# Optimization experiments

Measured on AMD Instinct MI355X. Metric: run time of the kernel, lower is better.

The kernel has to match this reference:

```python
import jax, jax.numpy as jnp
import numpy as np

GRID = (32, 32)       # SOM grid shape
INPUT_DIM = 512
BATCH = 16384
TAU = 0.5             # softmax temperature
EPS = 1e-8


def setup_inputs() -> dict:
    key = jax.random.key(0)
    k1, k2 = jax.random.split(key)
    x = jax.random.normal(k1, (BATCH, INPUT_DIM), dtype=jnp.float32)
    # glorot_uniform for shape (*GRID, INPUT_DIM): fan_in = 32*32, fan_out = 512
    fan_in, fan_out = GRID[0] * GRID[1], INPUT_DIM
    limit = float(np.sqrt(6.0 / (fan_in + fan_out)))
    weights_map = jax.random.uniform(
        k2, (*GRID, INPUT_DIM), dtype=jnp.float32, minval=-limit, maxval=limit
    )
    return {"x": x, "weights_map": weights_map}


def reference(x, weights_map):
    """SoftSOM forward: squared distances -> per-dimension softmax -> soft reconstruction."""
    B, D = x.shape
    gh, gw = GRID
    w_flat = weights_map.reshape(gh * gw, D)  # [N, D]
    d2 = (
        jnp.sum(x * x, axis=-1, keepdims=True)           # [B,1]
        + jnp.sum(w_flat * w_flat, axis=-1)[None, :]     # [1,N]
        - 2.0 * (x @ w_flat.T)                           # [B,N]
    )
    logits = (-d2 / TAU).reshape(B, gh, gw)
    # per-dimension softmax: softmax along each grid axis, combined multiplicatively
    s_rows = jax.nn.softmax(logits, axis=1)   # softmax over grid dim 0
    s_cols = jax.nn.softmax(logits, axis=2)   # softmax over grid dim 1
    a = s_rows * s_cols
    a = a / (jnp.sum(a, axis=(1, 2), keepdims=True) + EPS)  # renormalize over grid
    # soft reconstruction: weighted sum of prototypes
    y = jnp.einsum("bij,ijd->bd", a, weights_map)  # [B, D]
    return y
```

## Files before the change

### kernel.cpp

```cpp
#include <hip/hip_runtime.h>
#include <hip/hip_bf16.h>
#include <stdint.h>

#define B_SZ 16384
#define D_SZ 512
#define N_SZ 1024

using f16x8 = __attribute__((ext_vector_type(8))) _Float16;
using f32x4 = __attribute__((ext_vector_type(4))) float;

__device__ __forceinline__ unsigned short f16bits(_Float16 h) {
    return __builtin_bit_cast(unsigned short, h);
}

__global__ __launch_bounds__(256) void prep(
    const float* __restrict__ W, const float* __restrict__ X,
    _Float16* __restrict__ wh, _Float16* __restrict__ wt,
    float* __restrict__ ww, _Float16* __restrict__ xh) {
    const int bid = blockIdx.x;
    const int t = threadIdx.x;
    if (bid < 32) {
        __shared__ unsigned int cells[512 * 17];
        const int n0 = bid * 32;
        const int np = t >> 4;
        const int dc = t & 15;
        const int na = n0 + 2 * np, nb = na + 1;
        const int d0 = dc * 32;
        float va[32], vb[32];
#pragma unroll
        for (int i = 0; i < 8; ++i) {
            *reinterpret_cast<float4*>(&va[i * 4]) =
                *reinterpret_cast<const float4*>(&W[(size_t)na * D_SZ + d0 + i * 4]);
            *reinterpret_cast<float4*>(&vb[i * 4]) =
                *reinterpret_cast<const float4*>(&W[(size_t)nb * D_SZ + d0 + i * 4]);
        }
        float sa = 0.f, sb = 0.f;
#pragma unroll
        for (int i = 0; i < 32; ++i) { sa += va[i] * va[i]; sb += vb[i] * vb[i]; }
        sa += __shfl_xor(sa, 1); sa += __shfl_xor(sa, 2);
        sa += __shfl_xor(sa, 4); sa += __shfl_xor(sa, 8);
        sb += __shfl_xor(sb, 1); sb += __shfl_xor(sb, 2);
        sb += __shfl_xor(sb, 4); sb += __shfl_xor(sb, 8);
        if (dc == 0) { ww[na] = sa; ww[nb] = sb; }
        _Float16 ha[32], hb[32];
#pragma unroll
        for (int i = 0; i < 32; ++i) { ha[i] = (_Float16)va[i]; hb[i] = (_Float16)vb[i]; }
        unsigned int pa[16], pb[16];
#pragma unroll
        for (int j = 0; j < 16; ++j) {
            pa[j] = (unsigned)f16bits(ha[2 * j]) | ((unsigned)f16bits(ha[2 * j + 1]) << 16);
            pb[j] = (unsigned)f16bits(hb[2 * j]) | ((unsigned)f16bits(hb[2 * j + 1]) << 16);
        }
        unsigned int* whU = reinterpret_cast<unsigned int*>(wh);
#pragma unroll
        for (int j = 0; j < 4; ++j) {
            *reinterpret_cast<uint4*>(&whU[((size_t)na * D_SZ + d0) / 2 + j * 4]) =
                make_uint4(pa[j * 4], pa[j * 4 + 1], pa[j * 4 + 2], pa[j * 4 + 3]);
            *reinterpret_cast<uint4*>(&whU[((size_t)nb * D_SZ + d0) / 2 + j * 4]) =
                make_uint4(pb[j * 4], pb[j * 4 + 1], pb[j * 4 + 2], pb[j * 4 + 3]);
        }
#pragma unroll
        for (int k = 0; k < 32; ++k) {
            const int d = d0 + k;
            const unsigned u = (unsigned)f16bits(ha[k]) | ((unsigned)f16bits(hb[k]) << 16);
            cells[d * 17 + (np ^ ((d >> 5) & 15))] = u;
        }
        __syncthreads();
        for (int rr = 0; rr < 2; ++rr) {
            const int d = 2 * t + rr;
            const int px = (d >> 5) & 15;
            unsigned int buf[16];
#pragma unroll
            for (int j = 0; j < 16; ++j) buf[j] = cells[d * 17 + (j ^ px)];
            unsigned int* wtU = reinterpret_cast<unsigned int*>(wt);
#pragma unroll
            for (int j = 0; j < 4; ++j)
                *reinterpret_cast<uint4*>(&wtU[((size_t)d * N_SZ + n0) / 2 + j * 4]) =
                    make_uint4(buf[j * 4], buf[j * 4 + 1], buf[j * 4 + 2], buf[j * 4 + 3]);
        }
    } else {
        const int b2 = bid - 32;
        const int chunk = (b2 & 7) * 512 + (b2 >> 3);
        const size_t idx = ((size_t)chunk * 256 + t) * 8;
        const float4 a = *reinterpret_cast<const float4*>(&X[idx]);
        const float4 b = *reinterpret_cast<const float4*>(&X[idx + 4]);
        f16x8 h = {(_Float16)a.x, (_Float16)a.y, (_Float16)a.z, (_Float16)a.w,
                   (_Float16)b.x, (_Float16)b.y, (_Float16)b.z, (_Float16)b.w};
        *reinterpret_cast<f16x8*>(&xh[idx]) = h;
    }
}

__global__ __launch_bounds__(512, 2) void fused(
    const _Float16* __restrict__ xh, const _Float16* __restrict__ wh,
    const _Float16* __restrict__ wt, const float* __restrict__ ww,
    float* __restrict__ Y) {
    __shared__ __align__(16) char lds[152064];
    float* csw = (float*)lds;
    float* rs  = (float*)(lds + 131072);
    float* Mx  = (float*)(lds + 139264);
    float* Tw  = (float*)(lds + 141312);
    float* Mv  = (float*)(lds + 143360);
    float* Tv  = (float*)(lds + 143616);
    float* csf = (float*)(lds + 143872);

    const int tid = threadIdx.x;
    const int w = tid >> 6, l = tid & 63;
    const int l4 = l >> 4, lm = l & 15;
    const int raw = blockIdx.x;
    const int bm0 = ((raw & 7) * 32 + (raw >> 3)) * 64;

    f32x4 acc[4][8];
#pragma unroll
    for (int mi = 0; mi < 4; ++mi)
#pragma unroll
        for (int ni = 0; ni < 8; ++ni) acc[mi][ni] = (f32x4){0.f, 0.f, 0.f, 0.f};

    for (int kt = 0; kt < 16; ++kt) {
        const int gk = kt * 32;
        f16x8 af[4], bf[8];
#pragma unroll
        for (int mi = 0; mi < 4; ++mi)
            af[mi] = *reinterpret_cast<const f16x8*>(
                &xh[(size_t)(bm0 + mi * 16 + lm) * D_SZ + gk + l4 * 8]);
#pragma unroll
        for (int ni = 0; ni < 8; ++ni)
            bf[ni] = *reinterpret_cast<const f16x8*>(
                &wh[(size_t)(w * 128 + ni * 16 + lm) * D_SZ + gk + l4 * 8]);
#pragma unroll
        for (int mi = 0; mi < 4; ++mi)
#pragma unroll
            for (int ni = 0; ni < 8; ++ni)
                acc[mi][ni] = __builtin_amdgcn_mfma_f32_16x16x32_f16(af[mi], bf[ni], acc[mi][ni], 0, 0, 0);
    }
    float wwv[8];
#pragma unroll
    for (int ni = 0; ni < 8; ++ni) wwv[ni] = ww[w * 128 + ni * 16 + lm];
#pragma unroll
    for (int mi = 0; mi < 4; ++mi)
#pragma unroll
        for (int ni = 0; ni < 8; ++ni)
#pragma unroll
            for (int r = 0; r < 4; ++r)
                acc[mi][ni][r] = 4.f * acc[mi][ni][r] - 2.f * wwv[ni];

#pragma unroll
    for (int mi = 0; mi < 4; ++mi)
#pragma unroll
        for (int r = 0; r < 4; ++r) {
            float m = acc[mi][0][r];
#pragma unroll
            for (int ni = 1; ni < 8; ++ni) m = fmaxf(m, acc[mi][ni][r]);
            m = fmaxf(m, __shfl_xor(m, 1));
            m = fmaxf(m, __shfl_xor(m, 2));
            m = fmaxf(m, __shfl_xor(m, 4));
            m = fmaxf(m, __shfl_xor(m, 8));
            if (lm == 0) Mx[(mi * 16 + l4 * 4 + r) * 8 + w] = m;
        }
    __syncthreads();
    if (tid < 64) {
        float m = Mx[tid * 8];
#pragma unroll
        for (int k = 1; k < 8; ++k) m = fmaxf(m, Mx[tid * 8 + k]);
        Mv[tid] = m;
    }
    __syncthreads();
#pragma unroll
    for (int mi = 0; mi < 4; ++mi)
#pragma unroll
        for (int r = 0; r < 4; ++r) {
            const int b = mi * 16 + l4 * 4 + r;
            const float Mb = Mv[b];
            float u[8];
#pragma unroll
            for (int ni = 0; ni < 8; ++ni) {
                u[ni] = __expf(acc[mi][ni][r] - Mb);
                acc[mi][ni][r] = u[ni];
            }
#pragma unroll
            for (int ip = 0; ip < 4; ++ip) {
                float s = u[2 * ip] + u[2 * ip + 1];
                s += __shfl_xor(s, 1); s += __shfl_xor(s, 2);
                s += __shfl_xor(s, 4); s += __shfl_xor(s, 8);
                if (lm == 0) rs[b * 32 + 4 * w + ip] = s;
            }
#pragma unroll
            for (int jp = 0; jp < 2; ++jp) {
                const float c = (u[jp] + u[2 + jp]) + (u[4 + jp] + u[6 + jp]);
                csw[(w * 64 + b) * 32 + jp * 16 + lm] = c;
            }
        }
    __syncthreads();
    for (int c = tid; c < 2048; c += 512) {
        float s = csw[c];
#pragma unroll
        for (int k = 1; k < 8; ++k) s += csw[k * 2048 + c];
        csf[c] = s;
    }
    __syncthreads();
#pragma unroll
    for (int mi = 0; mi < 4; ++mi)
#pragma unroll
        for (int r = 0; r < 4; ++r) {
            const int b = mi * 16 + l4 * 4 + r;
            float rsv[4], csv[2];
#pragma unroll
            for (int ip = 0; ip < 4; ++ip) rsv[ip] = __builtin_amdgcn_rcpf(rs[b * 32 + 4 * w + ip]);
#pragma unroll
            for (int jp = 0; jp < 2; ++jp) csv[jp] = __builtin_amdgcn_rcpf(csf[b * 32 + jp * 16 + lm]);
            float tsum = 0.f;
#pragma unroll
            for (int ni = 0; ni < 8; ++ni) {
                const float uu = acc[mi][ni][r];
                const float t = uu * uu * rsv[ni >> 1] * csv[ni & 1];
                acc[mi][ni][r] = t;
                tsum += t;
            }
            tsum += __shfl_xor(tsum, 1); tsum += __shfl_xor(tsum, 2);
            tsum += __shfl_xor(tsum, 4); tsum += __shfl_xor(tsum, 8);
            if (lm == 0) Tw[b * 8 + w] = tsum;
        }
    __syncthreads();
    if (tid < 64) {
        float s = Tw[tid * 8];
#pragma unroll
        for (int k = 1; k < 8; ++k) s += Tw[tid * 8 + k];
        Tv[tid] = __builtin_amdgcn_rcpf(s + 1e-8f);
    }
    __syncthreads();
#pragma unroll
    for (int mi = 0; mi < 4; ++mi)
#pragma unroll
        for (int r = 0; r < 4; ++r) {
            const int b = mi * 16 + l4 * 4 + r;
            const float Tb = Tv[b];
#pragma unroll
            for (int ni = 0; ni < 8; ++ni) {
                const int n = w * 128 + ni * 16 + lm;
                const int off = b * 2048 + ((n * 2) ^ ((b & 7) << 4));
                *reinterpret_cast<_Float16*>(lds + off) = (_Float16)(acc[mi][ni][r] * Tb);
            }
        }
    __syncthreads();

    f32x4 acc2[4][4];
#pragma unroll
    for (int mi = 0; mi < 4; ++mi)
#pragma unroll
        for (int di = 0; di < 4; ++di) acc2[mi][di] = (f32x4){0.f, 0.f, 0.f, 0.f};

    for (int kt = 0; kt < 32; ++kt) {
        f16x8 a4[4], b4[4];
#pragma unroll
        for (int mi = 0; mi < 4; ++mi) {
            const int b = mi * 16 + lm;
            const int off = b * 2048 + ((kt * 64 + l4 * 16) ^ ((b & 7) << 4));
            a4[mi] = *reinterpret_cast<const f16x8*>(lds + off);
        }
#pragma unroll
        for (int di = 0; di < 4; ++di) {
            const int d = w * 64 + di * 16 + lm;
            b4[di] = *reinterpret_cast<const f16x8*>(
                &wt[(size_t)d * N_SZ + kt * 32 + l4 * 8]);
        }
#pragma unroll
        for (int mi = 0; mi < 4; ++mi)
#pragma unroll
            for (int di = 0; di < 4; ++di)
                acc2[mi][di] = __builtin_amdgcn_mfma_f32_16x16x32_f16(a4[mi], b4[di], acc2[mi][di], 0, 0, 0);
    }
#pragma unroll
    for (int mi = 0; mi < 4; ++mi)
#pragma unroll
        for (int di = 0; di < 4; ++di) {
            const int dd = w * 64 + di * 16 + lm;
            const int bb = bm0 + mi * 16 + l4 * 4;
#pragma unroll
            for (int r = 0; r < 4; ++r)
                Y[(size_t)(bb + r) * D_SZ + dd] = acc2[mi][di][r];
        }
}

extern "C" void kernel_launch(void* const* d_in, const int* in_sizes, int n_in,
                              void* d_out, int out_size, void* d_ws, size_t ws_size,
                              hipStream_t stream) {
    (void)in_sizes; (void)n_in; (void)out_size; (void)ws_size;
    const float* X = (const float*)d_in[0];
    const float* W = (const float*)d_in[1];
    float* Y = (float*)d_out;
    char* ws = (char*)d_ws;

    _Float16* wh = (_Float16*)ws;
    _Float16* wt = (_Float16*)(ws + (size_t)1 * 1024 * 1024);
    float*    ww = (float*)   (ws + (size_t)2 * 1024 * 1024);
    _Float16* xh = (_Float16*)(ws + (size_t)2 * 1024 * 1024 + 4096);

    prep<<<32 + 4096, 256, 0, stream>>>(W, X, wh, wt, ww, xh);
    fused<<<256, 512, 0, stream>>>(xh, wh, wt, ww, Y);
}
```

Baseline: 112.8 us.

## Halve row tile, stage swizzled X tile in LDS via direct global-to-LDS loads

The fused kernel's batch tile drops from 64 to 32 rows. The grid doubles to 512 blocks and LDS drops to about 76KB, so launch bounds rise to 4 waves-per-EU occupancy. The prep kernel now writes the fp16 X in an XOR-swizzled layout, and each block bulk-loads its X tile into LDS with global_load_lds before the first GEMM instead of reading it from global every k-step. The goal is more concurrency and latency hiding, at the cost of reloading W fragments from global twice as often per batch row.

```diff
diff --git a/kernel.cpp b/kernel.cpp
--- a/kernel.cpp
+++ b/kernel.cpp
@@ -8,6 +8,13 @@
 
 using f16x8 = __attribute__((ext_vector_type(8))) _Float16;
 using f32x4 = __attribute__((ext_vector_type(4))) float;
+
+typedef unsigned int u32_as1 __attribute__((address_space(1)));
+typedef unsigned int u32_as3 __attribute__((address_space(3)));
+
+__device__ __forceinline__ void gload16(const void* g, void* lds_base) {
+    __builtin_amdgcn_global_load_lds((const u32_as1*)g, (u32_as3*)lds_base, 16, 0, 0);
+}
 
 __device__ __forceinline__ unsigned short f16bits(_Float16 h) {
     return __builtin_bit_cast(unsigned short, h);
@@ -86,57 +93,77 @@
         const float4 b = *reinterpret_cast<const float4*>(&X[idx + 4]);
         f16x8 h = {(_Float16)a.x, (_Float16)a.y, (_Float16)a.z, (_Float16)a.w,
                    (_Float16)b.x, (_Float16)b.y, (_Float16)b.z, (_Float16)b.w};
-        *reinterpret_cast<f16x8*>(&xh[idx]) = h;
-    }
-}
-
-__global__ __launch_bounds__(512, 2) void fused(
-    const _Float16* __restrict__ xh, const _Float16* __restrict__ wh,
+        const size_t g0 = idx * 2;
+        const int row = (int)(idx >> 9);
+        const size_t gp = g0 ^ (size_t)((row & 7) << 4);
+        *reinterpret_cast<f16x8*>((char*)xh + gp) = h;
+    }
+}
+
+__global__ __launch_bounds__(512, 4) void fused(
+    const char* __restrict__ xhB, const _Float16* __restrict__ wh,
     const _Float16* __restrict__ wt, const float* __restrict__ ww,
     float* __restrict__ Y) {
-    __shared__ __align__(16) char lds[152064];
-    float* csw = (float*)lds;
-    float* rs  = (float*)(lds + 131072);
-    float* Mx  = (float*)(lds + 139264);
-    float* Tw  = (float*)(lds + 141312);
-    float* Mv  = (float*)(lds + 143360);
-    float* Tv  = (float*)(lds + 143616);
-    float* csf = (float*)(lds + 143872);
+    __shared__ __align__(16) char lds[76032];
+    float* csw = (float*)(lds + 32768);
+    float* rs  = (float*)(lds + 65536);
+    float* Mx  = (float*)(lds + 69632);
+    float* Tw  = (float*)(lds + 70656);
+    float* Mv  = (float*)(lds + 71680);
+    float* Tv  = (float*)(lds + 71808);
+    float* csf = (float*)(lds + 71936);
 
     const int tid = threadIdx.x;
     const int w = tid >> 6, l = tid & 63;
     const int l4 = l >> 4, lm = l & 15;
     const int raw = blockIdx.x;
-    const int bm0 = ((raw & 7) * 32 + (raw >> 3)) * 64;
-
-    f32x4 acc[4][8];
-#pragma unroll
-    for (int mi = 0; mi < 4; ++mi)
+    const int bm0 = ((raw & 7) * 64 + (raw >> 3)) * 32;
+
+    {
+        const size_t gbase = (size_t)bm0 * 1024;
+#pragma unroll
+        for (int s = 0; s < 4; ++s) {
+            const int off = s * 8192 + tid * 16;
+            gload16(xhB + gbase + off, lds + off);
+        }
+    }
+    __syncthreads();
+
+    f32x4 acc[2][8];
+#pragma unroll
+    for (int mi = 0; mi < 2; ++mi)
 #pragma unroll
         for (int ni = 0; ni < 8; ++ni) acc[mi][ni] = (f32x4){0.f, 0.f, 0.f, 0.f};
 
     for (int kt = 0; kt < 16; ++kt) {
         const int gk = kt * 32;
-        f16x8 af[4], bf[8];
-#pragma unroll
-        for (int mi = 0; mi < 4; ++mi)
-            af[mi] = *reinterpret_cast<const f16x8*>(
-                &xh[(size_t)(bm0 + mi * 16 + lm) * D_SZ + gk + l4 * 8]);
-#pragma unroll
-        for (int ni = 0; ni < 8; ++ni)
-            bf[ni] = *reinterpret_cast<const f16x8*>(
-                &wh[(size_t)(w * 128 + ni * 16 + lm) * D_SZ + gk + l4 * 8]);
-#pragma unroll
-        for (int mi = 0; mi < 4; ++mi)
-#pragma unroll
-            for (int ni = 0; ni < 8; ++ni)
-                acc[mi][ni] = __builtin_amdgcn_mfma_f32_16x16x32_f16(af[mi], bf[ni], acc[mi][ni], 0, 0, 0);
+        f16x8 af[2];
+#pragma unroll
+        for (int mi = 0; mi < 2; ++mi) {
+            const int r = mi * 16 + lm;
+            const int loff = (r * 1024 + gk * 2 + l4 * 16) ^ ((r & 7) << 4);
+            af[mi] = *reinterpret_cast<const f16x8*>(lds + loff);
+        }
+#pragma unroll
+        for (int nh = 0; nh < 2; ++nh) {
+            f16x8 bf[4];
+#pragma unroll
+            for (int nq = 0; nq < 4; ++nq)
+                bf[nq] = *reinterpret_cast<const f16x8*>(
+                    &wh[(size_t)(w * 128 + (nh * 4 + nq) * 16 + lm) * D_SZ + gk + l4 * 8]);
+#pragma unroll
+            for (int mi = 0; mi < 2; ++mi)
+#pragma unroll
+                for (int nq = 0; nq < 4; ++nq)
+                    acc[mi][nh * 4 + nq] = __builtin_amdgcn_mfma_f32_16x16x32_f16(
+                        af[mi], bf[nq], acc[mi][nh * 4 + nq], 0, 0, 0);
+        }
     }
     float wwv[8];
 #pragma unroll
     for (int ni = 0; ni < 8; ++ni) wwv[ni] = ww[w * 128 + ni * 16 + lm];
 #pragma unroll
-    for (int mi = 0; mi < 4; ++mi)
+    for (int mi = 0; mi < 2; ++mi)
 #pragma unroll
         for (int ni = 0; ni < 8; ++ni)
 #pragma unroll
@@ -144,7 +171,7 @@
                 acc[mi][ni][r] = 4.f * acc[mi][ni][r] - 2.f * wwv[ni];
 
 #pragma unroll
-    for (int mi = 0; mi < 4; ++mi)
+    for (int mi = 0; mi < 2; ++mi)
 #pragma unroll
         for (int r = 0; r < 4; ++r) {
             float m = acc[mi][0][r];
@@ -157,7 +184,7 @@
             if (lm == 0) Mx[(mi * 16 + l4 * 4 + r) * 8 + w] = m;
         }
     __syncthreads();
-    if (tid < 64) {
+    if (tid < 32) {
         float m = Mx[tid * 8];
 #pragma unroll
         for (int k = 1; k < 8; ++k) m = fmaxf(m, Mx[tid * 8 + k]);
@@ -165,7 +192,7 @@
     }
     __syncthreads();
 #pragma unroll
-    for (int mi = 0; mi < 4; ++mi)
+    for (int mi = 0; mi < 2; ++mi)
 #pragma unroll
         for (int r = 0; r < 4; ++r) {
             const int b = mi * 16 + l4 * 4 + r;
@@ -186,19 +213,19 @@
 #pragma unroll
             for (int jp = 0; jp < 2; ++jp) {
                 const float c = (u[jp] + u[2 + jp]) + (u[4 + jp] + u[6 + jp]);
-                csw[(w * 64 + b) * 32 + jp * 16 + lm] = c;
-            }
-        }
-    __syncthreads();
-    for (int c = tid; c < 2048; c += 512) {
+                csw[(w * 32 + b) * 32 + jp * 16 + lm] = c;
+            }
+        }
+    __syncthreads();
+    for (int c = tid; c < 1024; c += 512) {
         float s = csw[c];
 #pragma unroll
-        for (int k = 1; k < 8; ++k) s += csw[k * 2048 + c];
+        for (int k = 1; k < 8; ++k) s += csw[k * 1024 + c];
         csf[c] = s;
     }
     __syncthreads();
 #pragma unroll
-    for (int mi = 0; mi < 4; ++mi)
+    for (int mi = 0; mi < 2; ++mi)
 #pragma unroll
         for (int r = 0; r < 4; ++r) {
             const int b = mi * 16 + l4 * 4 + r;
@@ -220,7 +247,7 @@
             if (lm == 0) Tw[b * 8 + w] = tsum;
         }
     __syncthreads();
-    if (tid < 64) {
+    if (tid < 32) {
         float s = Tw[tid * 8];
 #pragma unroll
         for (int k = 1; k < 8; ++k) s += Tw[tid * 8 + k];
@@ -228,7 +255,7 @@
     }
     __syncthreads();
 #pragma unroll
-    for (int mi = 0; mi < 4; ++mi)
+    for (int mi = 0; mi < 2; ++mi)
 #pragma unroll
         for (int r = 0; r < 4; ++r) {
             const int b = mi * 16 + l4 * 4 + r;
@@ -242,16 +269,16 @@
         }
     __syncthreads();
 
-    f32x4 acc2[4][4];
-#pragma unroll
-    for (int mi = 0; mi < 4; ++mi)
+    f32x4 acc2[2][4];
+#pragma unroll
+    for (int mi = 0; mi < 2; ++mi)
 #pragma unroll
         for (int di = 0; di < 4; ++di) acc2[mi][di] = (f32x4){0.f, 0.f, 0.f, 0.f};
 
     for (int kt = 0; kt < 32; ++kt) {
-        f16x8 a4[4], b4[4];
-#pragma unroll
-        for (int mi = 0; mi < 4; ++mi) {
+        f16x8 a4[2], b4[4];
+#pragma unroll
+        for (int mi = 0; mi < 2; ++mi) {
             const int b = mi * 16 + lm;
             const int off = b * 2048 + ((kt * 64 + l4 * 16) ^ ((b & 7) << 4));
             a4[mi] = *reinterpret_cast<const f16x8*>(lds + off);
@@ -263,13 +290,13 @@
                 &wt[(size_t)d * N_SZ + kt * 32 + l4 * 8]);
         }
 #pragma unroll
-        for (int mi = 0; mi < 4; ++mi)
+        for (int mi = 0; mi < 2; ++mi)
 #pragma unroll
             for (int di = 0; di < 4; ++di)
                 acc2[mi][di] = __builtin_amdgcn_mfma_f32_16x16x32_f16(a4[mi], b4[di], acc2[mi][di], 0, 0, 0);
     }
 #pragma unroll
-    for (int mi = 0; mi < 4; ++mi)
+    for (int mi = 0; mi < 2; ++mi)
 #pragma unroll
         for (int di = 0; di < 4; ++di) {
             const int dd = w * 64 + di * 16 + lm;
@@ -295,5 +322,5 @@
     _Float16* xh = (_Float16*)(ws + (size_t)2 * 1024 * 1024 + 4096);
 
     prep<<<32 + 4096, 256, 0, stream>>>(W, X, wh, wt, ww, xh);
-    fused<<<256, 512, 0, stream>>>(xh, wh, wt, ww, Y);
-}
+    fused<<<512, 512, 0, stream>>>((const char*)xh, wh, wt, ww, Y);
+}
```

After: 139.4 us. +23.5%, slower.
